# Kernel optimization log

Measured on AMD Instinct MI355X. Metric: run time of the kernel, lower is better.

The kernel has to match this reference:

```python
import jax, jax.numpy as jnp
import numpy as np

B, S, D = 4, 2048, 1024
E = 8           # num_experts
TOP_K = 2
H = 3 * D       # hidden_mult = 3


def setup_inputs() -> dict:
    key = jax.random.key(0)
    ks = jax.random.split(key, 5)
    scale_d = 1.0 / np.sqrt(D)
    scale_h = 1.0 / np.sqrt(H)
    return {
        "x": jax.random.normal(ks[0], (B, S, D), dtype=jnp.float32),
        "gate_w": jax.random.normal(ks[1], (D, E), dtype=jnp.float32) * scale_d,
        "w1": jax.random.normal(ks[2], (E, D, H), dtype=jnp.float32) * scale_d,
        "w3": jax.random.normal(ks[3], (E, D, H), dtype=jnp.float32) * scale_d,
        "w2": jax.random.normal(ks[4], (E, H, D), dtype=jnp.float32) * scale_h,
    }


def reference(x, gate_w, w1, w2, w3):
    b, s, d = x.shape
    t = b * s
    xf = x.reshape(t, d)                                  # [T, D]
    probs = jax.nn.softmax(xf @ gate_w, axis=-1)          # [T, E]
    vals, idx = jax.lax.top_k(probs, TOP_K)               # [T, K]
    w = vals / jnp.sum(vals, axis=-1, keepdims=True)      # renormalized top-k weights
    # per-token combine weight for each expert (scatter top-k weights)
    comb = jnp.zeros((t, E), dtype=x.dtype).at[
        jnp.arange(t)[:, None], idx
    ].add(w)                                              # [T, E]
    out = jnp.zeros_like(xf)
    for e in range(E):  # small fixed expert count
        h = jax.nn.silu(xf @ w1[e]) * (xf @ w3[e])        # [T, H] SwiGLU
        out = out + comb[:, e:e + 1] * (h @ w2[e])        # weighted combine
    return out.reshape(b, s, d)
```

## Files before the change

### kernel.cpp

```cpp
#include <hip/hip_runtime.h>
#include <stdint.h>

#define T_TOK 8192
#define DDIM 1024
#define NEXP 8
#define HDIM 3072

typedef __attribute__((ext_vector_type(8))) short bfrag;
typedef __attribute__((ext_vector_type(4))) float facc;

__device__ __forceinline__ void gload16(const void* g, void* l) {
  __builtin_amdgcn_global_load_lds(
      (const __attribute__((address_space(1))) void*)g,
      (__attribute__((address_space(3))) void*)l, 16, 0, 0);
}

__device__ __forceinline__ unsigned short f2bf(float f) {
  unsigned int u = __float_as_uint(f);
  u += 0x7FFFu + ((u >> 16) & 1u);
  return (unsigned short)(u >> 16);
}

__global__ void calc_offs(const int* __restrict__ counts, int* __restrict__ offs,
                          int* __restrict__ t1e, int* __restrict__ t1p,
                          int* __restrict__ t2e, int* __restrict__ t2p)
{
  if (threadIdx.x == 0 && blockIdx.x == 0) {
    int a = 0;
#pragma unroll
    for (int e = 0; e < NEXP; ++e) { offs[e] = a; a += counts[e * 32]; }
    offs[NEXP] = a;
    int nb = 0;
    for (int e = 0; e < NEXP; ++e) {
      const int c = counts[e * 32];
      for (int p = 0; p < c; p += 128) { t1e[nb] = e; t1p[nb] = p; ++nb; }
    }
    offs[9] = nb;
    nb = 0;
    for (int e = 0; e < NEXP; ++e) {
      const int c = counts[e * 32];
      for (int p = 0; p < c; p += 128) { t2e[nb] = e; t2p[nb] = p; ++nb; }
    }
    offs[10] = nb;
  }
}

__device__ __forceinline__ void conv_tile(
    const float* __restrict__ se, unsigned short* __restrict__ de,
    int K, int N, int k0, int n0)
{
  __shared__ unsigned short Tb[64][130];
  const int tid = threadIdx.x;
#pragma unroll
  for (int i = 0; i < 8; ++i) {
    const int f = i * 256 + tid;
    const int kl = f >> 5, nq = (f & 31) * 4;
    const float4 v = *(const float4*)(se + (size_t)(k0 + kl) * N + n0 + nq);
    Tb[kl][nq + 0] = f2bf(v.x);
    Tb[kl][nq + 1] = f2bf(v.y);
    Tb[kl][nq + 2] = f2bf(v.z);
    Tb[kl][nq + 3] = f2bf(v.w);
  }
  __syncthreads();
#pragma unroll
  for (int i = 0; i < 4; ++i) {
    const int idx = i * 256 + tid;
    const int n = idx >> 3, up = idx & 7;
    const int kb = (up ^ (n & 7)) * 8;
    union { unsigned short s[8]; uint4 v; } t;
#pragma unroll
    for (int j = 0; j < 8; ++j) t.s[j] = Tb[kb + j][n];
    *(uint4*)(de + ((size_t)(n0 + n) * K + k0 + up * 8)) = t.v;
  }
}

__global__ __launch_bounds__(256) void convert_gate(
    const float* __restrict__ w1, const float* __restrict__ w3,
    const float* __restrict__ w2, unsigned short* __restrict__ w1t,
    unsigned short* __restrict__ w3t, unsigned short* __restrict__ w2t,
    const float* __restrict__ x, const float* __restrict__ gw,
    int* __restrict__ counts, int* __restrict__ tok_list,
    float* __restrict__ wt_list, int* __restrict__ slotA,
    int* __restrict__ slotB, unsigned short* __restrict__ xb)
{
  const int g = blockIdx.x;
  if (g < 9216) {
    const int seg = g / 3072, r = g % 3072;
    const int e = r / 384, rr = r % 384;
    if (seg < 2) {
      const float* src = (seg == 0 ? w1 : w3) + (size_t)e * DDIM * HDIM;
      unsigned short* dst = (seg == 0 ? w1t : w3t) + (size_t)e * HDIM * DDIM;
      conv_tile(src, dst, DDIM, HDIM, (rr / 24) * 64, (rr % 24) * 128);
    } else {
      conv_tile(w2 + (size_t)e * HDIM * DDIM, w2t + (size_t)e * DDIM * HDIM,
                HDIM, DDIM, (rr / 8) * 64, (rr % 8) * 128);
    }
    return;
  }
  const int lane = threadIdx.x & 63;
  const int t = (g - 9216) * 4 + (threadIdx.x >> 6);
  const float* xr = x + (size_t)t * DDIM;
  unsigned short* xbr = xb + (size_t)t * DDIM;
  float p[NEXP];
#pragma unroll
  for (int e = 0; e < NEXP; ++e) p[e] = 0.f;
#pragma unroll 4
  for (int i = 0; i < DDIM / 64; ++i) {
    const int d = i * 64 + lane;
    const float xv = xr[d];
    xbr[d] = f2bf(xv);
    const float4 g0 = *(const float4*)(gw + (size_t)d * NEXP);
    const float4 g1 = *(const float4*)(gw + (size_t)d * NEXP + 4);
    p[0] += xv * g0.x; p[1] += xv * g0.y; p[2] += xv * g0.z; p[3] += xv * g0.w;
    p[4] += xv * g1.x; p[5] += xv * g1.y; p[6] += xv * g1.z; p[7] += xv * g1.w;
  }
#pragma unroll
  for (int off = 32; off > 0; off >>= 1) {
#pragma unroll
    for (int e = 0; e < NEXP; ++e) p[e] += __shfl_down(p[e], off);
  }
  if (lane == 0) {
    int i1 = 0; float v1 = p[0];
#pragma unroll
    for (int e = 1; e < NEXP; ++e) if (p[e] > v1) { v1 = p[e]; i1 = e; }
    int i2 = -1; float v2 = -3.4e38f;
#pragma unroll
    for (int e = 0; e < NEXP; ++e) if (e != i1 && p[e] > v2) { v2 = p[e]; i2 = e; }
    const float w0 = 1.f / (1.f + __expf(v2 - v1));
    int q1 = atomicAdd(&counts[i1 * 32], 1);
    tok_list[i1 * T_TOK + q1] = t;
    wt_list[i1 * T_TOK + q1] = w0;
    slotA[t] = i1 * T_TOK + q1;
    int q2 = atomicAdd(&counts[i2 * 32], 1);
    tok_list[i2 * T_TOK + q2] = t;
    wt_list[i2 * T_TOK + q2] = 1.f - w0;
    slotB[t] = i2 * T_TOK + q2;
  }
}

__global__ __launch_bounds__(256, 2) void moe_gemm1(
    const unsigned short* __restrict__ xb, const unsigned short* __restrict__ w1t,
    const unsigned short* __restrict__ w3t, const int* __restrict__ counts,
    const int* __restrict__ offs, const int* __restrict__ t1e,
    const int* __restrict__ t1p, const int* __restrict__ tok_list,
    unsigned short* __restrict__ h_buf)
{
  const int b = blockIdx.y;
  if (b >= offs[9]) return;
  const int e = t1e[b];
  const int p0 = t1p[b];
  const int cnt = counts[e * 32];
  const int n0 = blockIdx.x * 64;
  const int hbase = offs[e];

  __shared__ __align__(16) unsigned short As[128 * 64];
  __shared__ __align__(16) unsigned short B1s[64 * 64];
  __shared__ __align__(16) unsigned short B3s[64 * 64];

  const int tid = threadIdx.x;
  const int lane = tid & 63;
  const int wv = tid >> 6;
  const int wm = wv >> 1;
  const int wn = wv & 1;
  const int lr = lane & 15;
  const int lg = lane >> 4;
  const int l8 = lane >> 3;
  const int lu = lane & 7;
  const int aswz = (lu ^ l8) * 16;

  const int* tl = tok_list + e * T_TOK;

  const unsigned short* asrc[4];
#pragma unroll
  for (int i = 0; i < 4; ++i) {
    const int p = p0 + wv * 32 + i * 8 + l8;
    const int tok = (p < cnt) ? tl[p] : 0;
    asrc[i] = xb + (size_t)tok * DDIM;
  }
  const unsigned short* b1src[2];
  const unsigned short* b3src[2];
#pragma unroll
  for (int i = 0; i < 2; ++i) {
    const int n = n0 + wv * 16 + i * 8 + l8;
    b1src[i] = w1t + (size_t)(e * HDIM + n) * DDIM;
    b3src[i] = w3t + (size_t)(e * HDIM + n) * DDIM;
  }

  facc acc1[4][2], acc3[4][2];
#pragma unroll
  for (int m = 0; m < 4; ++m)
#pragma unroll
    for (int n = 0; n < 2; ++n)
#pragma unroll
      for (int q = 0; q < 4; ++q) { acc1[m][n][q] = 0.f; acc3[m][n][q] = 0.f; }

#pragma unroll 1
  for (int k0 = 0; k0 < DDIM; k0 += 64) {
#pragma unroll
    for (int i = 0; i < 4; ++i)
      gload16((const char*)asrc[i] + k0 * 2 + aswz, &As[(wv * 4 + i) * 512]);
#pragma unroll
    for (int i = 0; i < 2; ++i) {
      gload16((const char*)b1src[i] + k0 * 2 + lu * 16, &B1s[(wv * 2 + i) * 512]);
      gload16((const char*)b3src[i] + k0 * 2 + lu * 16, &B3s[(wv * 2 + i) * 512]);
    }
    __syncthreads();
#pragma unroll
    for (int ks = 0; ks < 2; ++ks) {
      bfrag a[4];
#pragma unroll
      for (int m = 0; m < 4; ++m) {
        const int r = wm * 64 + m * 16 + lr;
        const int u = (ks * 4 + lg) ^ (r & 7);
        a[m] = *(const bfrag*)&As[r * 64 + u * 8];
      }
#pragma unroll
      for (int n = 0; n < 2; ++n) {
        const int rb = wn * 32 + n * 16 + lr;
        const int u = (ks * 4 + lg) ^ (rb & 7);
        const bfrag b1 = *(const bfrag*)&B1s[rb * 64 + u * 8];
#pragma unroll
        for (int m = 0; m < 4; ++m)
          acc1[m][n] = __builtin_amdgcn_mfma_f32_16x16x32_bf16(a[m], b1, acc1[m][n], 0, 0, 0);
        const bfrag b3 = *(const bfrag*)&B3s[rb * 64 + u * 8];
#pragma unroll
        for (int m = 0; m < 4; ++m)
          acc3[m][n] = __builtin_amdgcn_mfma_f32_16x16x32_bf16(a[m], b3, acc3[m][n], 0, 0, 0);
      }
    }
    __syncthreads();
  }

#pragma unroll
  for (int m = 0; m < 4; ++m)
#pragma unroll
    for (int n = 0; n < 2; ++n)
#pragma unroll
      for (int q = 0; q < 4; ++q) {
        const float a1 = acc1[m][n][q];
        const float a3 = acc3[m][n][q];
        const float hv = a1 * a3 / (1.f + __expf(-a1));
        const int row = wm * 64 + m * 16 + lg * 4 + q;
        const int col = wn * 32 + n * 16 + lr;
        As[row * 64 + col] = f2bf(hv);
      }
  __syncthreads();
#pragma unroll
  for (int i = 0; i < 4; ++i) {
    const int idx = i * 256 + tid;
    const int r = idx >> 3, u = idx & 7;
    if (p0 + r < cnt)
      *(uint4*)(h_buf + ((size_t)(hbase + p0 + r) * HDIM + n0 + u * 8)) =
          *(const uint4*)&As[r * 64 + u * 8];
  }
}

__global__ __launch_bounds__(256, 2) void moe_gemm2(
    const unsigned short* __restrict__ h_buf, const unsigned short* __restrict__ w2t,
    const int* __restrict__ counts, const int* __restrict__ offs,
    const int* __restrict__ t2e, const int* __restrict__ t2p,
    float* __restrict__ part)
{
  const int b = blockIdx.y;
  if (b >= offs[10]) return;
  const int e = t2e[b];
  const int p0 = t2p[b];
  const int cnt = counts[e * 32];
  const int n0 = blockIdx.x * 128;
  const int hbase = offs[e];

  __shared__ __align__(16) unsigned short Ah[128 * 64];
  __shared__ __align__(16) unsigned short Bw[128 * 64];

  const int tid = threadIdx.x;
  const int lane = tid & 63;
  const int wv = tid >> 6;
  const int wm = wv >> 1;
  const int wn = wv & 1;
  const int lr = lane & 15;
  const int lg = lane >> 4;
  const int l8 = lane >> 3;
  const int lu = lane & 7;
  const int aswz = (lu ^ l8) * 16;

  const unsigned short* asrc[4];
#pragma unroll
  for (int i = 0; i < 4; ++i) {
    const int p = p0 + wv * 32 + i * 8 + l8;
    const int hrow = hbase + ((p < cnt) ? p : 0);
    asrc[i] = h_buf + (size_t)hrow * HDIM;
  }
  const unsigned short* bsrc[4];
#pragma unroll
  for (int i = 0; i < 4; ++i) {
    const int n = n0 + wv * 32 + i * 8 + l8;
    bsrc[i] = w2t + (size_t)(e * DDIM + n) * HDIM;
  }

  facc acc[4][4];
#pragma unroll
  for (int m = 0; m < 4; ++m)
#pragma unroll
    for (int n = 0; n < 4; ++n)
#pragma unroll
      for (int q = 0; q < 4; ++q) acc[m][n][q] = 0.f;

#pragma unroll 1
  for (int k0 = 0; k0 < HDIM; k0 += 64) {
#pragma unroll
    for (int i = 0; i < 4; ++i)
      gload16((const char*)asrc[i] + k0 * 2 + aswz, &Ah[(wv * 4 + i) * 512]);
#pragma unroll
    for (int i = 0; i < 4; ++i)
      gload16((const char*)bsrc[i] + k0 * 2 + lu * 16, &Bw[(wv * 4 + i) * 512]);
    __syncthreads();
#pragma unroll
    for (int ks = 0; ks < 2; ++ks) {
      bfrag a[4];
#pragma unroll
      for (int m = 0; m < 4; ++m) {
        const int r = wm * 64 + m * 16 + lr;
        const int u = (ks * 4 + lg) ^ (r & 7);
        a[m] = *(const bfrag*)&Ah[r * 64 + u * 8];
      }
#pragma unroll
      for (int n = 0; n < 4; ++n) {
        const int rb = wn * 64 + n * 16 + lr;
        const int u = (ks * 4 + lg) ^ (rb & 7);
        const bfrag bb = *(const bfrag*)&Bw[rb * 64 + u * 8];
#pragma unroll
        for (int m = 0; m < 4; ++m)
          acc[m][n] = __builtin_amdgcn_mfma_f32_16x16x32_bf16(a[m], bb, acc[m][n], 0, 0, 0);
      }
    }
    __syncthreads();
  }

#pragma unroll
  for (int m = 0; m < 4; ++m)
#pragma unroll
    for (int q = 0; q < 4; ++q) {
      const int p = p0 + wm * 64 + m * 16 + lg * 4 + q;
      if (p < cnt) {
        float* dst = part + (size_t)(hbase + p) * DDIM + n0 + wn * 64 + lr;
#pragma unroll
        for (int n = 0; n < 4; ++n)
          dst[n * 16] = acc[m][n][q];
      }
    }
}

__global__ __launch_bounds__(256) void combine_out(
    const float* __restrict__ part, const int* __restrict__ slotA,
    const int* __restrict__ slotB, const float* __restrict__ wt_list,
    const int* __restrict__ offs, float* __restrict__ out)
{
  const int t = blockIdx.x;
  const int sA = slotA[t], sB = slotB[t];
  const float wA = wt_list[sA], wB = wt_list[sB];
  const int pA = offs[sA >> 13] + (sA & (T_TOK - 1));
  const int pB = offs[sB >> 13] + (sB & (T_TOK - 1));
  const float* ra = part + (size_t)pA * DDIM;
  const float* rb = part + (size_t)pB * DDIM;
  float* o = out + (size_t)t * DDIM;
  const int i = threadIdx.x * 4;
  const float4 a = *(const float4*)(ra + i);
  const float4 b = *(const float4*)(rb + i);
  float4 r;
  r.x = wA * a.x + wB * b.x;
  r.y = wA * a.y + wB * b.y;
  r.z = wA * a.z + wB * b.z;
  r.w = wA * a.w + wB * b.w;
  *(float4*)(o + i) = r;
}

__global__ __launch_bounds__(64) void gate_topk_fb(
    const float* __restrict__ x, const float* __restrict__ gw,
    int* __restrict__ counts, int* __restrict__ tok_list,
    float* __restrict__ wt_list)
{
  const int t = blockIdx.x;
  const int lane = threadIdx.x;
  const float* xr = x + (size_t)t * DDIM;
  float p[NEXP];
#pragma unroll
  for (int e = 0; e < NEXP; ++e) p[e] = 0.f;
#pragma unroll 4
  for (int i = 0; i < DDIM / 64; ++i) {
    const int d = i * 64 + lane;
    const float xv = xr[d];
    const float4 g0 = *(const float4*)(gw + (size_t)d * NEXP);
    const float4 g1 = *(const float4*)(gw + (size_t)d * NEXP + 4);
    p[0] += xv * g0.x; p[1] += xv * g0.y; p[2] += xv * g0.z; p[3] += xv * g0.w;
    p[4] += xv * g1.x; p[5] += xv * g1.y; p[6] += xv * g1.z; p[7] += xv * g1.w;
  }
#pragma unroll
  for (int off = 32; off > 0; off >>= 1) {
#pragma unroll
    for (int e = 0; e < NEXP; ++e) p[e] += __shfl_down(p[e], off);
  }
  if (lane == 0) {
    int i1 = 0; float v1 = p[0];
#pragma unroll
    for (int e = 1; e < NEXP; ++e) if (p[e] > v1) { v1 = p[e]; i1 = e; }
    int i2 = -1; float v2 = -3.4e38f;
#pragma unroll
    for (int e = 0; e < NEXP; ++e) if (e != i1 && p[e] > v2) { v2 = p[e]; i2 = e; }
    const float w0 = 1.f / (1.f + __expf(v2 - v1));
    int q1 = atomicAdd(&counts[i1 * 32], 1);
    tok_list[i1 * T_TOK + q1] = t;
    wt_list[i1 * T_TOK + q1] = w0;
    int q2 = atomicAdd(&counts[i2 * 32], 1);
    tok_list[i2 * T_TOK + q2] = t;
    wt_list[i2 * T_TOK + q2] = 1.f - w0;
  }
}

__global__ __launch_bounds__(256) void moe_gemm1_fb(
    const float* __restrict__ x, const float* __restrict__ w1,
    const float* __restrict__ w3, const int* __restrict__ counts,
    const int* __restrict__ tok_list, unsigned short* __restrict__ h_buf,
    int e)
{
  const int cnt = counts[e * 32];
  const int p0 = blockIdx.y * 64;
  if (p0 >= cnt) return;
  const int n0 = blockIdx.x * 64;

  __shared__ unsigned short As[64][40];
  __shared__ unsigned short B1s[64][40];
  __shared__ unsigned short B3s[64][40];

  const int tid = threadIdx.x;
  const int lane = tid & 63;
  const int wv = tid >> 6;

  const float* w1e = w1 + (size_t)e * DDIM * HDIM;
  const float* w3e = w3 + (size_t)e * DDIM * HDIM;
  const int* tl = tok_list + e * T_TOK;

  const int arow = tid >> 2;
  const int akseg = (tid & 3) * 8;
  int tok = -1;
  if (p0 + arow < cnt) tok = tl[p0 + arow];

  const int bk = tid >> 3;
  const int bn4 = (tid & 7) * 4;

  facc acc1[4], acc3[4];
#pragma unroll
  for (int i = 0; i < 4; ++i)
#pragma unroll
    for (int j = 0; j < 4; ++j) { acc1[i][j] = 0.f; acc3[i][j] = 0.f; }

  const int mrow = wv * 16 + (lane & 15);
  const int kq = (lane >> 4) * 8;

  for (int k0 = 0; k0 < DDIM; k0 += 32) {
    {
      union { unsigned short s[8]; uint4 v; } tmp;
      if (tok >= 0) {
        const float* src = x + (size_t)tok * DDIM + k0 + akseg;
        const float4 f0 = *(const float4*)(src);
        const float4 f1 = *(const float4*)(src + 4);
        tmp.s[0]=f2bf(f0.x); tmp.s[1]=f2bf(f0.y); tmp.s[2]=f2bf(f0.z); tmp.s[3]=f2bf(f0.w);
        tmp.s[4]=f2bf(f1.x); tmp.s[5]=f2bf(f1.y); tmp.s[6]=f2bf(f1.z); tmp.s[7]=f2bf(f1.w);
      } else {
        tmp.v = make_uint4(0u, 0u, 0u, 0u);
      }
      *(uint4*)&As[arow][akseg] = tmp.v;
    }
#pragma unroll
    for (int pass = 0; pass < 2; ++pass) {
      const int n = bn4 + pass * 32;
      const float4 f1v = *(const float4*)(w1e + (size_t)(k0 + bk) * HDIM + n0 + n);
      B1s[n + 0][bk] = f2bf(f1v.x);
      B1s[n + 1][bk] = f2bf(f1v.y);
      B1s[n + 2][bk] = f2bf(f1v.z);
      B1s[n + 3][bk] = f2bf(f1v.w);
      const float4 f3v = *(const float4*)(w3e + (size_t)(k0 + bk) * HDIM + n0 + n);
      B3s[n + 0][bk] = f2bf(f3v.x);
      B3s[n + 1][bk] = f2bf(f3v.y);
      B3s[n + 2][bk] = f2bf(f3v.z);
      B3s[n + 3][bk] = f2bf(f3v.w);
    }
    __syncthreads();
    const bfrag a = *(const bfrag*)&As[mrow][kq];
#pragma unroll
    for (int nt = 0; nt < 4; ++nt) {
      const bfrag b1 = *(const bfrag*)&B1s[nt * 16 + (lane & 15)][kq];
      acc1[nt] = __builtin_amdgcn_mfma_f32_16x16x32_bf16(a, b1, acc1[nt], 0, 0, 0);
      const bfrag b3 = *(const bfrag*)&B3s[nt * 16 + (lane & 15)][kq];
      acc3[nt] = __builtin_amdgcn_mfma_f32_16x16x32_bf16(a, b3, acc3[nt], 0, 0, 0);
    }
    __syncthreads();
  }
  const int rbase = p0 + wv * 16 + ((lane >> 4) * 4);
  const int cbase = n0 + (lane & 15);
#pragma unroll
  for (int r = 0; r < 4; ++r) {
    const int p = rbase + r;
    if (p < cnt) {
      unsigned short* dst = h_buf + (size_t)p * HDIM + cbase;
#pragma unroll
      for (int nt = 0; nt < 4; ++nt) {
        const float a1 = acc1[nt][r];
        const float a3 = acc3[nt][r];
        const float hv = a1 * a3 / (1.f + __expf(-a1));
        dst[nt * 16] = f2bf(hv);
      }
    }
  }
}

__global__ __launch_bounds__(256) void moe_gemm2_fb(
    const unsigned short* __restrict__ h_buf, const float* __restrict__ w2,
    const int* __restrict__ counts, const int* __restrict__ tok_list,
    const float* __restrict__ wt_list, float* __restrict__ out, int e)
{
  const int cnt = counts[e * 32];
  const int p0 = blockIdx.y * 64;
  if (p0 >= cnt) return;
  const int n0 = blockIdx.x * 64;

  __shared__ unsigned short As[64][40];
  __shared__ unsigned short Bs[64][40];

  const int tid = threadIdx.x;
  const int lane = tid & 63;
  const int wv = tid >> 6;

  const float* w2e = w2 + (size_t)e * HDIM * DDIM;
  const int* tl = tok_list + e * T_TOK;
  const float* wl = wt_list + e * T_TOK;

  const int arow = tid >> 2;
  const int akseg = (tid & 3) * 8;
  const bool avalid = (p0 + arow < cnt);

  const int bk = tid >> 3;
  const int bn4 = (tid & 7) * 4;

  facc acc[4];
#pragma unroll
  for (int i = 0; i < 4; ++i)
#pragma unroll
    for (int j = 0; j < 4; ++j) acc[i][j] = 0.f;

  const int mrow = wv * 16 + (lane & 15);
  const int kq = (lane >> 4) * 8;

  for (int k0 = 0; k0 < HDIM; k0 += 32) {
    if (avalid) {
      *(uint4*)&As[arow][akseg] =
          *(const uint4*)(h_buf + (size_t)(p0 + arow) * HDIM + k0 + akseg);
    } else {
      *(uint4*)&As[arow][akseg] = make_uint4(0u, 0u, 0u, 0u);
    }
#pragma unroll
    for (int pass = 0; pass < 2; ++pass) {
      const int n = bn4 + pass * 32;
      const float4 f = *(const float4*)(w2e + (size_t)(k0 + bk) * DDIM + n0 + n);
      Bs[n + 0][bk] = f2bf(f.x);
      Bs[n + 1][bk] = f2bf(f.y);
      Bs[n + 2][bk] = f2bf(f.z);
      Bs[n + 3][bk] = f2bf(f.w);
    }
    __syncthreads();
    const bfrag a = *(const bfrag*)&As[mrow][kq];
#pragma unroll
    for (int nt = 0; nt < 4; ++nt) {
      const bfrag b = *(const bfrag*)&Bs[nt * 16 + (lane & 15)][kq];
      acc[nt] = __builtin_amdgcn_mfma_f32_16x16x32_bf16(a, b, acc[nt], 0, 0, 0);
    }
    __syncthreads();
  }
  const int rbase = p0 + wv * 16 + ((lane >> 4) * 4);
  const int cbase = n0 + (lane & 15);
#pragma unroll
  for (int r = 0; r < 4; ++r) {
    const int p = rbase + r;
    if (p < cnt) {
      const int tok = tl[p];
      const float wt = wl[p];
      float* dst = out + (size_t)tok * DDIM + cbase;
#pragma unroll
      for (int nt = 0; nt < 4; ++nt) {
        atomicAdd(dst + nt * 16, acc[nt][r] * wt);
      }
    }
  }
}

__global__ void ws_too_small(float* out, int n) {
  int i = blockIdx.x * 256 + threadIdx.x;
  if (i < n) out[i] = 1.0e6f;
}

extern "C" void kernel_launch(void* const* d_in, const int* in_sizes, int n_in,
                              void* d_out, int out_size, void* d_ws, size_t ws_size,
                              hipStream_t stream) {
  const float* x  = (const float*)d_in[0];
  const float* gw = (const float*)d_in[1];
  const float* w1 = (const float*)d_in[2];
  const float* w3 = (const float*)d_in[3];
  const float* w2 = (const float*)d_in[4];
  float* out = (float*)d_out;

  const size_t off_tok = 5120;
  const size_t off_wt  = off_tok + (size_t)NEXP * T_TOK * 4;
  const size_t off_sA  = off_wt + (size_t)NEXP * T_TOK * 4;
  const size_t off_sB  = off_sA + (size_t)T_TOK * 4;
  const size_t off_xb  = off_sB + (size_t)T_TOK * 4;
  const size_t off_w1t = off_xb + (size_t)T_TOK * DDIM * 2;
  const size_t off_w3t = off_w1t + (size_t)NEXP * DDIM * HDIM * 2;
  const size_t off_w2t = off_w3t + (size_t)NEXP * DDIM * HDIM * 2;
  const size_t off_h   = off_w2t + (size_t)NEXP * HDIM * DDIM * 2;
  const size_t need    = off_h + (size_t)(2 * T_TOK) * HDIM * 2;
  const size_t off_part = off_w1t;

  if (ws_size >= need) {
    int* counts = (int*)d_ws;
    int* offs = (int*)((char*)d_ws + 1024);
    int* t1e = (int*)((char*)d_ws + 2048);
    int* t1p = (int*)((char*)d_ws + 2688);
    int* t2e = (int*)((char*)d_ws + 3328);
    int* t2p = (int*)((char*)d_ws + 3968);
    int* tok_list = (int*)((char*)d_ws + off_tok);
    float* wt_list = (float*)((char*)d_ws + off_wt);
    int* slotA = (int*)((char*)d_ws + off_sA);
    int* slotB = (int*)((char*)d_ws + off_sB);
    unsigned short* xb  = (unsigned short*)((char*)d_ws + off_xb);
    unsigned short* w1t = (unsigned short*)((char*)d_ws + off_w1t);
    unsigned short* w3t = (unsigned short*)((char*)d_ws + off_w3t);
    unsigned short* w2t = (unsigned short*)((char*)d_ws + off_w2t);
    unsigned short* h_buf = (unsigned short*)((char*)d_ws + off_h);
    float* part = (float*)((char*)d_ws + off_part);

    hipMemsetAsync(counts, 0, 1024, stream);

    convert_gate<<<9216 + T_TOK / 4, 256, 0, stream>>>(
        w1, w3, w2, w1t, w3t, w2t, x, gw, counts, tok_list, wt_list,
        slotA, slotB, xb);
    calc_offs<<<1, 1, 0, stream>>>(counts, offs, t1e, t1p, t2e, t2p);
    moe_gemm1<<<dim3(HDIM / 64, 144), 256, 0, stream>>>(
        xb, w1t, w3t, counts, offs, t1e, t1p, tok_list, h_buf);
    moe_gemm2<<<dim3(DDIM / 128, 144), 256, 0, stream>>>(
        h_buf, w2t, counts, offs, t2e, t2p, part);
    combine_out<<<T_TOK, 256, 0, stream>>>(part, slotA, slotB, wt_list, offs, out);
    return;
  }

  const size_t fb_off_tok = 1024;
  const size_t fb_off_wt  = fb_off_tok + (size_t)NEXP * T_TOK * 4;
  const size_t fb_off_h   = fb_off_wt + (size_t)NEXP * T_TOK * 4;
  const size_t fb_need    = fb_off_h + (size_t)T_TOK * HDIM * 2;
  if (ws_size < fb_need) {
    ws_too_small<<<(out_size + 255) / 256, 256, 0, stream>>>(out, out_size);
    return;
  }
  int* counts = (int*)d_ws;
  int* tok_list = (int*)((char*)d_ws + fb_off_tok);
  float* wt_list = (float*)((char*)d_ws + fb_off_wt);
  unsigned short* h_buf = (unsigned short*)((char*)d_ws + fb_off_h);

  hipMemsetAsync(counts, 0, 1024, stream);
  hipMemsetAsync(out, 0, (size_t)out_size * sizeof(float), stream);

  gate_topk_fb<<<T_TOK, 64, 0, stream>>>(x, gw, counts, tok_list, wt_list);
  for (int e = 0; e < NEXP; ++e) {
    moe_gemm1_fb<<<dim3(HDIM / 64, T_TOK / 64), 256, 0, stream>>>(
        x, w1, w3, counts, tok_list, h_buf, e);
    moe_gemm2_fb<<<dim3(DDIM / 64, T_TOK / 64), 256, 0, stream>>>(
        h_buf, w2, counts, tok_list, wt_list, out, e);
  }
}
```

Baseline: 718.1 us.

## Rewrite gate/up GEMM with 256x128 tiles, double-buffered LDS and interleaved prefetch

Replaces the first expert GEMM kernel with a 512-thread version using 256-token by 128-column tiles for both w1 and w3, with 128 KB of double-buffered LDS. Global-to-LDS loads for the next K step are interleaved with MFMA phases, using explicit vmcnt waits, barriers and setprio. The aim is to hide load latency and raise data reuse per tile. The epilogue stages fp32 accumulators through LDS before applying SiLU, and the tile bookkeeping moves to 256-row steps. This risks lower occupancy from the large LDS footprint and more padding waste on small experts.

```diff
diff --git a/kernel.cpp b/kernel.cpp
--- a/kernel.cpp
+++ b/kernel.cpp
@@ -33,7 +33,7 @@
     int nb = 0;
     for (int e = 0; e < NEXP; ++e) {
       const int c = counts[e * 32];
-      for (int p = 0; p < c; p += 128) { t1e[nb] = e; t1p[nb] = p; ++nb; }
+      for (int p = 0; p < c; p += 256) { t1e[nb] = e; t1p[nb] = p; ++nb; }
     }
     offs[9] = nb;
     nb = 0;
@@ -138,7 +138,7 @@
   }
 }
 
-__global__ __launch_bounds__(256, 2) void moe_gemm1(
+__global__ __launch_bounds__(512, 2) void moe_gemm1(
     const unsigned short* __restrict__ xb, const unsigned short* __restrict__ w1t,
     const unsigned short* __restrict__ w3t, const int* __restrict__ counts,
     const int* __restrict__ offs, const int* __restrict__ t1e,
@@ -150,12 +150,179 @@
   const int e = t1e[b];
   const int p0 = t1p[b];
   const int cnt = counts[e * 32];
-  const int n0 = blockIdx.x * 64;
+  const int n0 = blockIdx.x * 128;
   const int hbase = offs[e];
 
-  __shared__ __align__(16) unsigned short As[128 * 64];
-  __shared__ __align__(16) unsigned short B1s[64 * 64];
-  __shared__ __align__(16) unsigned short B3s[64 * 64];
+  __shared__ __align__(16) unsigned short lds[65536];
+
+  const int tid = threadIdx.x;
+  const int lane = tid & 63;
+  const int wv = tid >> 6;
+  const int lr = lane & 15;
+  const int lg = lane >> 4;
+  const int srow = tid >> 3;
+  const int sunit = tid & 7;
+  const int aswz = (sunit ^ (srow & 7)) * 16;
+
+  const int* tl = tok_list + e * T_TOK;
+
+  const char* aps[4];
+#pragma unroll
+  for (int h = 0; h < 2; ++h)
+#pragma unroll
+    for (int L = 0; L < 2; ++L) {
+      const int p = p0 + h * 128 + L * 64 + srow;
+      const int tok = (p < cnt) ? tl[p] : 0;
+      aps[h * 2 + L] = (const char*)(xb + (size_t)tok * DDIM) + aswz;
+    }
+  const char* bps[4];
+#pragma unroll
+  for (int h = 0; h < 2; ++h)
+#pragma unroll
+    for (int L = 0; L < 2; ++L) {
+      const unsigned short* base = h ? w3t : w1t;
+      bps[h * 2 + L] =
+          (const char*)(base + (size_t)(e * HDIM + n0 + L * 64 + srow) * DDIM)
+          + sunit * 16;
+    }
+
+  facc acc[4][4][2];
+#pragma unroll
+  for (int q = 0; q < 4; ++q)
+#pragma unroll
+    for (int m = 0; m < 4; ++m)
+#pragma unroll
+      for (int n = 0; n < 2; ++n)
+#pragma unroll
+        for (int j = 0; j < 4; ++j) acc[q][m][n][j] = 0.f;
+
+  bfrag bb[2][2];
+  bfrag a_[4][2];
+
+#define FENCE asm volatile("" ::: "memory")
+#define SB __builtin_amdgcn_s_barrier()
+#define SCHB __builtin_amdgcn_sched_barrier(0)
+#define VMW(n) asm volatile("s_waitcnt vmcnt(" #n ")" ::: "memory")
+
+#define STGA(s, h, kt)                                                         \
+  { gload16(aps[(h) * 2 + 0] + (size_t)(kt) * 128,                             \
+            &lds[(s) * 16384 + (h) * 8192 + srow * 64 + sunit * 8]);           \
+    gload16(aps[(h) * 2 + 1] + (size_t)(kt) * 128,                             \
+            &lds[(s) * 16384 + (h) * 8192 + (64 + srow) * 64 + sunit * 8]); }
+#define STGB(s, h, kt)                                                         \
+  { gload16(bps[(h) * 2 + 0] + (size_t)(kt) * 128,                             \
+            &lds[32768 + (s) * 16384 + (h) * 8192 + srow * 64 + sunit * 8]);   \
+    gload16(bps[(h) * 2 + 1] + (size_t)(kt) * 128,                             \
+            &lds[32768 + (s) * 16384 + (h) * 8192 + (64 + srow) * 64 + sunit * 8]); }
+
+#define LOADB(s)                                                               \
+  _Pragma("unroll") for (int n = 0; n < 2; ++n)                                \
+  _Pragma("unroll") for (int ks = 0; ks < 2; ++ks) {                           \
+    const int rb = wv * 32 + n * 16 + lr;                                      \
+    const int u = (ks * 4 + lg) ^ (lr & 7);                                    \
+    bb[n][ks] = *(const bfrag*)&lds[32768 + (s) * 16384 + rb * 64 + u * 8];    \
+  }
+
+#define PH(s, q, STG, WAITS)                                                   \
+  {                                                                            \
+    _Pragma("unroll") for (int m = 0; m < 4; ++m)                              \
+    _Pragma("unroll") for (int ks = 0; ks < 2; ++ks) {                         \
+      const int r = (q) * 64 + m * 16 + lr;                                    \
+      const int u = (ks * 4 + lg) ^ (lr & 7);                                  \
+      a_[m][ks] = *(const bfrag*)&lds[(s) * 16384 + r * 64 + u * 8];           \
+    }                                                                          \
+    STG;                                                                       \
+    FENCE; SB; SCHB;                                                           \
+    __builtin_amdgcn_s_setprio(1);                                             \
+    _Pragma("unroll") for (int ks = 0; ks < 2; ++ks)                           \
+    _Pragma("unroll") for (int n = 0; n < 2; ++n)                              \
+    _Pragma("unroll") for (int m = 0; m < 4; ++m)                              \
+      acc[q][m][n] = __builtin_amdgcn_mfma_f32_16x16x32_bf16(                  \
+          a_[m][ks], bb[n][ks], acc[q][m][n], 0, 0, 0);                        \
+    __builtin_amdgcn_s_setprio(0);                                             \
+    WAITS;                                                                     \
+    FENCE; SB; SCHB;                                                           \
+  }
+
+  STGB(0, 0, 0); STGB(0, 1, 0); STGA(0, 0, 0); STGA(0, 1, 0); STGA(1, 0, 1);
+  VMW(2); FENCE; SB; SCHB;
+
+#pragma unroll 1
+  for (int t = 0; t < 8; ++t) {
+    const int k1 = 2 * t + 1, k2 = 2 * t + 2, k3 = 2 * t + 3;
+    LOADB(0);
+    PH(0, 0, STGB(1, 0, k1), );
+    PH(0, 1, STGB(1, 1, k1), );
+    PH(0, 2, STGA(1, 1, k1), );
+    PH(0, 3, STGA(0, 0, k2), VMW(4));
+    LOADB(1);
+    PH(1, 0, STGA(0, 1, k2), );
+    PH(1, 1, STGB(0, 0, k2), VMW(6));
+    PH(1, 2, STGB(0, 1, k2), );
+    PH(1, 3, STGA(1, 0, k3), VMW(2));
+  }
+
+  VMW(0); FENCE;
+  __syncthreads();
+
+  float* Lf = (float*)lds;
+#pragma unroll
+  for (int P = 0; P < 2; ++P) {
+    if (P) __syncthreads();
+#pragma unroll
+    for (int qq = 0; qq < 2; ++qq)
+#pragma unroll
+      for (int m = 0; m < 4; ++m)
+#pragma unroll
+        for (int n = 0; n < 2; ++n)
+#pragma unroll
+          for (int rg = 0; rg < 4; ++rg)
+            Lf[(qq * 64 + m * 16 + lg * 4 + rg) * 256 + wv * 32 + n * 16 + lr] =
+                acc[P * 2 + qq][m][n][rg];
+    __syncthreads();
+#pragma unroll
+    for (int it = 0; it < 4; ++it) {
+      const int idx = it * 512 + tid;
+      const int r = idx >> 4, u = idx & 15;
+      const int p = p0 + P * 128 + r;
+      if (p < cnt) {
+        union { unsigned short s[8]; uint4 v; } o;
+#pragma unroll
+        for (int j = 0; j < 8; ++j) {
+          const float l = Lf[r * 256 + u * 8 + j];
+          const float gg = Lf[r * 256 + 128 + u * 8 + j];
+          o.s[j] = f2bf(l * gg / (1.f + __expf(-l)));
+        }
+        *(uint4*)(h_buf + ((size_t)(hbase + p) * HDIM + n0 + u * 8)) = o.v;
+      }
+    }
+  }
+#undef PH
+#undef LOADB
+#undef STGA
+#undef STGB
+#undef VMW
+#undef SCHB
+#undef SB
+#undef FENCE
+}
+
+__global__ __launch_bounds__(256, 2) void moe_gemm2(
+    const unsigned short* __restrict__ h_buf, const unsigned short* __restrict__ w2t,
+    const int* __restrict__ counts, const int* __restrict__ offs,
+    const int* __restrict__ t2e, const int* __restrict__ t2p,
+    float* __restrict__ part)
+{
+  const int b = blockIdx.y;
+  if (b >= offs[10]) return;
+  const int e = t2e[b];
+  const int p0 = t2p[b];
+  const int cnt = counts[e * 32];
+  const int n0 = blockIdx.x * 128;
+  const int hbase = offs[e];
+
+  __shared__ __align__(16) unsigned short Ah[128 * 64];
+  __shared__ __align__(16) unsigned short Bw[128 * 64];
 
   const int tid = threadIdx.x;
   const int lane = tid & 63;
@@ -168,121 +335,6 @@
   const int lu = lane & 7;
   const int aswz = (lu ^ l8) * 16;
 
-  const int* tl = tok_list + e * T_TOK;
-
-  const unsigned short* asrc[4];
-#pragma unroll
-  for (int i = 0; i < 4; ++i) {
-    const int p = p0 + wv * 32 + i * 8 + l8;
-    const int tok = (p < cnt) ? tl[p] : 0;
-    asrc[i] = xb + (size_t)tok * DDIM;
-  }
-  const unsigned short* b1src[2];
-  const unsigned short* b3src[2];
-#pragma unroll
-  for (int i = 0; i < 2; ++i) {
-    const int n = n0 + wv * 16 + i * 8 + l8;
-    b1src[i] = w1t + (size_t)(e * HDIM + n) * DDIM;
-    b3src[i] = w3t + (size_t)(e * HDIM + n) * DDIM;
-  }
-
-  facc acc1[4][2], acc3[4][2];
-#pragma unroll
-  for (int m = 0; m < 4; ++m)
-#pragma unroll
-    for (int n = 0; n < 2; ++n)
-#pragma unroll
-      for (int q = 0; q < 4; ++q) { acc1[m][n][q] = 0.f; acc3[m][n][q] = 0.f; }
-
-#pragma unroll 1
-  for (int k0 = 0; k0 < DDIM; k0 += 64) {
-#pragma unroll
-    for (int i = 0; i < 4; ++i)
-      gload16((const char*)asrc[i] + k0 * 2 + aswz, &As[(wv * 4 + i) * 512]);
-#pragma unroll
-    for (int i = 0; i < 2; ++i) {
-      gload16((const char*)b1src[i] + k0 * 2 + lu * 16, &B1s[(wv * 2 + i) * 512]);
-      gload16((const char*)b3src[i] + k0 * 2 + lu * 16, &B3s[(wv * 2 + i) * 512]);
-    }
-    __syncthreads();
-#pragma unroll
-    for (int ks = 0; ks < 2; ++ks) {
-      bfrag a[4];
-#pragma unroll
-      for (int m = 0; m < 4; ++m) {
-        const int r = wm * 64 + m * 16 + lr;
-        const int u = (ks * 4 + lg) ^ (r & 7);
-        a[m] = *(const bfrag*)&As[r * 64 + u * 8];
-      }
-#pragma unroll
-      for (int n = 0; n < 2; ++n) {
-        const int rb = wn * 32 + n * 16 + lr;
-        const int u = (ks * 4 + lg) ^ (rb & 7);
-        const bfrag b1 = *(const bfrag*)&B1s[rb * 64 + u * 8];
-#pragma unroll
-        for (int m = 0; m < 4; ++m)
-          acc1[m][n] = __builtin_amdgcn_mfma_f32_16x16x32_bf16(a[m], b1, acc1[m][n], 0, 0, 0);
-        const bfrag b3 = *(const bfrag*)&B3s[rb * 64 + u * 8];
-#pragma unroll
-        for (int m = 0; m < 4; ++m)
-          acc3[m][n] = __builtin_amdgcn_mfma_f32_16x16x32_bf16(a[m], b3, acc3[m][n], 0, 0, 0);
-      }
-    }
-    __syncthreads();
-  }
-
-#pragma unroll
-  for (int m = 0; m < 4; ++m)
-#pragma unroll
-    for (int n = 0; n < 2; ++n)
-#pragma unroll
-      for (int q = 0; q < 4; ++q) {
-        const float a1 = acc1[m][n][q];
-        const float a3 = acc3[m][n][q];
-        const float hv = a1 * a3 / (1.f + __expf(-a1));
-        const int row = wm * 64 + m * 16 + lg * 4 + q;
-        const int col = wn * 32 + n * 16 + lr;
-        As[row * 64 + col] = f2bf(hv);
-      }
-  __syncthreads();
-#pragma unroll
-  for (int i = 0; i < 4; ++i) {
-    const int idx = i * 256 + tid;
-    const int r = idx >> 3, u = idx & 7;
-    if (p0 + r < cnt)
-      *(uint4*)(h_buf + ((size_t)(hbase + p0 + r) * HDIM + n0 + u * 8)) =
-          *(const uint4*)&As[r * 64 + u * 8];
-  }
-}
-
-__global__ __launch_bounds__(256, 2) void moe_gemm2(
-    const unsigned short* __restrict__ h_buf, const unsigned short* __restrict__ w2t,
-    const int* __restrict__ counts, const int* __restrict__ offs,
-    const int* __restrict__ t2e, const int* __restrict__ t2p,
-    float* __restrict__ part)
-{
-  const int b = blockIdx.y;
-  if (b >= offs[10]) return;
-  const int e = t2e[b];
-  const int p0 = t2p[b];
-  const int cnt = counts[e * 32];
-  const int n0 = blockIdx.x * 128;
-  const int hbase = offs[e];
-
-  __shared__ __align__(16) unsigned short Ah[128 * 64];
-  __shared__ __align__(16) unsigned short Bw[128 * 64];
-
-  const int tid = threadIdx.x;
-  const int lane = tid & 63;
-  const int wv = tid >> 6;
-  const int wm = wv >> 1;
-  const int wn = wv & 1;
-  const int lr = lane & 15;
-  const int lg = lane >> 4;
-  const int l8 = lane >> 3;
-  const int lu = lane & 7;
-  const int aswz = (lu ^ l8) * 16;
-
   const unsigned short* asrc[4];
 #pragma unroll
   for (int i = 0; i < 4; ++i) {
@@ -327,10 +379,10 @@
       for (int n = 0; n < 4; ++n) {
         const int rb = wn * 64 + n * 16 + lr;
         const int u = (ks * 4 + lg) ^ (rb & 7);
-        const bfrag bb = *(const bfrag*)&Bw[rb * 64 + u * 8];
+        const bfrag bbv = *(const bfrag*)&Bw[rb * 64 + u * 8];
 #pragma unroll
         for (int m = 0; m < 4; ++m)
-          acc[m][n] = __builtin_amdgcn_mfma_f32_16x16x32_bf16(a[m], bb, acc[m][n], 0, 0, 0);
+          acc[m][n] = __builtin_amdgcn_mfma_f32_16x16x32_bf16(a[m], bbv, acc[m][n], 0, 0, 0);
       }
     }
     __syncthreads();
@@ -643,7 +695,7 @@
         w1, w3, w2, w1t, w3t, w2t, x, gw, counts, tok_list, wt_list,
         slotA, slotB, xb);
     calc_offs<<<1, 1, 0, stream>>>(counts, offs, t1e, t1p, t2e, t2p);
-    moe_gemm1<<<dim3(HDIM / 64, 144), 256, 0, stream>>>(
+    moe_gemm1<<<dim3(HDIM / 128, 72), 512, 0, stream>>>(
         xb, w1t, w3t, counts, offs, t1e, t1p, tok_list, h_buf);
     moe_gemm2<<<dim3(DDIM / 128, 144), 256, 0, stream>>>(
         h_buf, w2t, counts, offs, t2e, t2p, part);
```

New measurement: 759.0 us. 5.7% more time.
